# Optimization experiments

Hardware: AMD Instinct MI355X
Metric: run time of the kernel (lower is better)

The kernel has to match this reference:

```python
import jax, jax.numpy as jnp
import numpy as np

B, L = 2048, 8192
IN, H, OUT = 128, 512, 10
N_FRAMES = L // IN  # frame_step == frame_size -> non-overlapping unfold == reshape


def _lstm_layer(xs, W_ih, W_hh, b):
    """xs: [T, B, D_in]; returns (hs [T, B, H], h_T [B, H]).
    PyTorch gate order: i, f, g, o."""
    Bsz = xs.shape[1]
    h0 = jnp.zeros((Bsz, H), xs.dtype)
    c0 = jnp.zeros((Bsz, H), xs.dtype)

    def step(carry, x_t):
        h, c = carry
        gates = x_t @ W_ih.T + h @ W_hh.T + b  # [B, 4H]
        i, f, g, o = jnp.split(gates, 4, axis=-1)
        c = jax.nn.sigmoid(f) * c + jax.nn.sigmoid(i) * jnp.tanh(g)
        h = jax.nn.sigmoid(o) * jnp.tanh(c)
        return (h, c), h

    (hT, _), hs = jax.lax.scan(step, (h0, c0), xs)
    return hs, hT


def setup_inputs() -> dict:
    key = jax.random.key(0)
    ks = jax.random.split(key, 12)
    s_in = 1.0 / np.sqrt(H)
    return {
        "xb": jax.random.normal(ks[0], (B, L), jnp.float32),
        "W_ih0": jax.random.normal(ks[1], (4 * H, IN), jnp.float32) * s_in,
        "W_hh0": jax.random.normal(ks[2], (4 * H, H), jnp.float32) * s_in,
        "b0": jax.random.normal(ks[3], (4 * H,), jnp.float32) * s_in,
        "W_ih1": jax.random.normal(ks[4], (4 * H, H), jnp.float32) * s_in,
        "W_hh1": jax.random.normal(ks[5], (4 * H, H), jnp.float32) * s_in,
        "b1": jax.random.normal(ks[6], (4 * H,), jnp.float32) * s_in,
        "W_out": jax.random.normal(ks[7], (OUT, H), jnp.float32) * s_in,
        "b_out": jax.random.normal(ks[8], (OUT,), jnp.float32) * s_in,
    }


def reference(xb, W_ih0, W_hh0, b0, W_ih1, W_hh1, b1, W_out, b_out):
    # unfold(1, fs, fs) with step==size -> reshape; transpose to time-major
    frames = xb.reshape(B, N_FRAMES, IN).transpose(1, 0, 2)  # [T, B, IN]
    hs0, _ = _lstm_layer(frames, W_ih0, W_hh0, b0)           # [T, B, H]
    _, hT1 = _lstm_layer(hs0, W_ih1, W_hh1, b1)              # [B, H]
    return hT1 @ W_out.T + b_out                             # [B, OUT]
```

## Files before the change

kernel.cpp:

```cpp
#include <hip/hip_runtime.h>
#include <hip/hip_bf16.h>


typedef _Float16 f16x8 __attribute__((ext_vector_type(8)));
typedef float f32x4 __attribute__((ext_vector_type(4)));

#define Bsz 2048
#define Lsz 8192
#define Tsz 64

__global__ void cvt_f32_f16(const float* __restrict__ src, _Float16* __restrict__ dst, int n4) {
    int stride = gridDim.x * blockDim.x;
    for (int i = blockIdx.x * blockDim.x + threadIdx.x; i < n4; i += stride) {
        float4 v = ((const float4*)src)[i];
        union { _Float16 h[4]; ushort4 u; } o;
        o.h[0] = (_Float16)v.x; o.h[1] = (_Float16)v.y;
        o.h[2] = (_Float16)v.z; o.h[3] = (_Float16)v.w;
        ((ushort4*)dst)[i] = o.u;
    }
}

__global__ void pack_w(const float* __restrict__ Wih, const float* __restrict__ Whh,
                       _Float16* __restrict__ dst, int K1) {
    int KT = K1 + 512;
    int n4 = 2048 * KT / 4;
    int stride = gridDim.x * blockDim.x;
    for (int i = blockIdx.x * blockDim.x + threadIdx.x; i < n4; i += stride) {
        int row = i / (KT / 4);
        int col = (i % (KT / 4)) * 4;
        const float* s = (col < K1) ? (Wih + (size_t)row * K1 + col)
                                    : (Whh + (size_t)row * 512 + (col - K1));
        float4 v = *(const float4*)s;
        union { _Float16 h[4]; ushort4 u; } o;
        o.h[0] = (_Float16)v.x; o.h[1] = (_Float16)v.y;
        o.h[2] = (_Float16)v.z; o.h[3] = (_Float16)v.w;
        ((ushort4*)dst)[i] = o.u;
    }
}

__device__ __forceinline__ float fsig(float x)  { return 1.0f / (1.0f + __expf(-x)); }
__device__ __forceinline__ float ftanh(float x) { return 1.0f - 2.0f / (__expf(2.0f * x) + 1.0f); }

template<int K1>
__device__ __forceinline__ void step_tile_lds(
    const _Float16* __restrict__ A1, int lda1,
    const _Float16* __restrict__ A2,
    const _Float16* __restrict__ Wcat,
    const float* __restrict__ bias,
    float* __restrict__ c,
    _Float16* __restrict__ h_out,
    int rowblk, int hcb, char* lA, char* lB)
{
    constexpr int KT  = K1 + 512;
    constexpr int NIT = KT / 64;
    const int tid = threadIdx.x;
    const int ln  = tid & 63;
    const int wv  = tid >> 6;
    const int llo = ln & 15, lhi = ln >> 4;
    const int wx  = wv & 1,  wy  = wv >> 1;
    const int hc0 = hcb * 32;
    const int col = hc0 + wy * 16 + llo;

    const int rsub = ln >> 3;
    const int cg8  = ((ln & 7) ^ rsub) * 8;

    f32x4 acc[4][4] = {};

    float bz[4];
#pragma unroll
    for (int g = 0; g < 4; ++g) bz[g] = bias[512 * g + col];

    for (int it = 0; it < NIT; ++it) {
        const int k0 = it * 64;
#pragma unroll
        for (int q = 0; q < 4; ++q) {
            const int row  = wv * 32 + q * 8 + rsub;
            const int kcol = k0 + cg8;
            const int brow = rowblk * 128 + row;
            const _Float16* srcA = (kcol < K1)
                ? (A1 + (size_t)brow * lda1 + kcol)
                : (A2 + (size_t)brow * 512 + (kcol - K1));
            __builtin_amdgcn_global_load_lds(
                (const __attribute__((address_space(1))) void*)srcA,
                (__attribute__((address_space(3))) void*)(lA + wv * 4096 + q * 1024),
                16, 0, 0);
            const int wrow = ((row >> 5) << 9) + hc0 + (row & 31);
            const _Float16* srcB = Wcat + (size_t)wrow * KT + kcol;
            __builtin_amdgcn_global_load_lds(
                (const __attribute__((address_space(1))) void*)srcB,
                (__attribute__((address_space(3))) void*)(lB + wv * 4096 + q * 1024),
                16, 0, 0);
        }
        __syncthreads();

#pragma unroll
        for (int ks = 0; ks < 2; ++ks) {
            const int gsw = (((ks * 4 + lhi) ^ (llo & 7)) << 4);
            f16x8 a[4], b[4];
#pragma unroll
            for (int mi = 0; mi < 4; ++mi)
                a[mi] = *(const f16x8*)(lA + (wx * 64 + 16 * mi + llo) * 128 + gsw);
#pragma unroll
            for (int g = 0; g < 4; ++g)
                b[g] = *(const f16x8*)(lB + (g * 32 + wy * 16 + llo) * 128 + gsw);
#pragma unroll
            for (int g = 0; g < 4; ++g)
#pragma unroll
                for (int mi = 0; mi < 4; ++mi)
                    acc[g][mi] = __builtin_amdgcn_mfma_f32_16x16x32_f16(
                        a[mi], b[g], acc[g][mi], 0, 0, 0);
        }
        __syncthreads();
    }

#pragma unroll
    for (int mi = 0; mi < 4; ++mi) {
#pragma unroll
        for (int r = 0; r < 4; ++r) {
            const int row = rowblk * 128 + wx * 64 + 16 * mi + lhi * 4 + r;
            float iv = acc[0][mi][r] + bz[0];
            float fv = acc[1][mi][r] + bz[1];
            float gv = acc[2][mi][r] + bz[2];
            float ov = acc[3][mi][r] + bz[3];
            size_t idx = (size_t)row * 512 + col;
            float co = c[idx];
            float cn = fsig(fv) * co + fsig(iv) * ftanh(gv);
            float hn = fsig(ov) * ftanh(cn);
            c[idx] = cn;
            h_out[idx] = (_Float16)hn;
        }
    }
}

__global__ __launch_bounds__(256, 2) void lstm_round(
    int t0, int t1,
    const _Float16* __restrict__ xb16,
    const _Float16* __restrict__ Wc0, const float* __restrict__ b0, float* __restrict__ c0,
    _Float16* __restrict__ h00, _Float16* __restrict__ h01,
    const _Float16* __restrict__ Wc1, const float* __restrict__ b1, float* __restrict__ c1,
    _Float16* __restrict__ h10, _Float16* __restrict__ h11)
{
    __shared__ __align__(16) char lA[16384];
    __shared__ __align__(16) char lB[16384];
    const int bid    = blockIdx.x;
    const int gr     = bid & 7;
    const int rowblk = (bid >> 3) & 15;
    const int gq     = bid >> 7;
    const int grp    = gq * 8 + gr;
    const int hcb    = grp & 15;

    if (grp < 16) {
        if (t0 < 0) return;
        const _Float16* hr = (t0 & 1) ? h01 : h00;
        _Float16*       hw = (t0 & 1) ? h00 : h01;
        step_tile_lds<128>(xb16 + (size_t)t0 * 128, Lsz, hr, Wc0, b0, c0, hw, rowblk, hcb, lA, lB);
    } else {
        if (t1 < 0) return;
        const _Float16* h0in = ((t1 + 1) & 1) ? h01 : h00;
        const _Float16* hr   = (t1 & 1) ? h11 : h10;
        _Float16*       hw   = (t1 & 1) ? h10 : h11;
        step_tile_lds<512>(h0in, 512, hr, Wc1, b1, c1, hw, rowblk, hcb, lA, lB);
    }
}

__global__ void proj_kernel(const _Float16* __restrict__ h1,
                            const float* __restrict__ Wout,
                            const float* __restrict__ bout,
                            float* __restrict__ out)
{
    int tid = blockIdx.x * blockDim.x + threadIdx.x;
    if (tid >= Bsz * 10) return;
    int b = tid / 10, o = tid % 10;
    float s = bout[o];
    const _Float16* hrow = h1 + (size_t)b * 512;
    const float* wrow = Wout + (size_t)o * 512;
    for (int k = 0; k < 512; ++k) s += (float)hrow[k] * wrow[k];
    out[tid] = s;
}

extern "C" void kernel_launch(void* const* d_in, const int* in_sizes, int n_in,
                              void* d_out, int out_size, void* d_ws, size_t ws_size,
                              hipStream_t stream) {
    const float* xb    = (const float*)d_in[0];
    const float* W_ih0 = (const float*)d_in[1];
    const float* W_hh0 = (const float*)d_in[2];
    const float* b0    = (const float*)d_in[3];
    const float* W_ih1 = (const float*)d_in[4];
    const float* W_hh1 = (const float*)d_in[5];
    const float* b1    = (const float*)d_in[6];
    const float* W_out = (const float*)d_in[7];
    const float* b_out = (const float*)d_in[8];
    float* out = (float*)d_out;

    char* ws = (char*)d_ws;
    size_t off = 0;
    auto alloc = [&](size_t bytes) -> void* {
        void* p = ws + off;
        off += (bytes + 255) & ~(size_t)255;
        return p;
    };
    _Float16* xb16 = (_Float16*)alloc((size_t)Bsz * Lsz * 2);
    _Float16* Wc0  = (_Float16*)alloc((size_t)2048 * 640 * 2);
    _Float16* Wc1  = (_Float16*)alloc((size_t)2048 * 1024 * 2);
    _Float16* h00  = (_Float16*)alloc((size_t)Bsz * 512 * 2);
    _Float16* h01  = (_Float16*)alloc((size_t)Bsz * 512 * 2);
    _Float16* h10  = (_Float16*)alloc((size_t)Bsz * 512 * 2);
    _Float16* h11  = (_Float16*)alloc((size_t)Bsz * 512 * 2);
    float* c0 = (float*)alloc((size_t)Bsz * 512 * 4);
    float* c1 = (float*)alloc((size_t)Bsz * 512 * 4);

    cvt_f32_f16<<<2048, 256, 0, stream>>>(xb, xb16, Bsz * Lsz / 4);
    pack_w<<<1280, 256, 0, stream>>>(W_ih0, W_hh0, Wc0, 128);
    pack_w<<<2048, 256, 0, stream>>>(W_ih1, W_hh1, Wc1, 512);

    hipMemsetAsync(h00, 0, (size_t)Bsz * 512 * 2, stream);
    hipMemsetAsync(h10, 0, (size_t)Bsz * 512 * 2, stream);
    hipMemsetAsync(c0, 0, (size_t)Bsz * 512 * 4, stream);
    hipMemsetAsync(c1, 0, (size_t)Bsz * 512 * 4, stream);

    for (int r = 0; r <= Tsz; ++r) {
        int t0 = (r < Tsz) ? r : -1;
        int t1 = r - 1;
        lstm_round<<<dim3(512), 256, 0, stream>>>(t0, t1,
            xb16, Wc0, b0, c0, h00, h01,
            Wc1, b1, c1, h10, h11);
    }

    proj_kernel<<<(Bsz * 10 + 255) / 256, 256, 0, stream>>>(h10, W_out, b_out, out);
}
```

Baseline: 1.784 ms.

## Retile LSTM step to 64x512 blocks with double-buffered LDS and LDS-staged epilogue

Each block now computes a 64-row by 512-gate-column tile (all four gates for 128 hidden units) using 512 threads, instead of 128x128 tiles with 256 threads. K-tile staging is double-buffered in a 144 KB LDS allocation, so the next tile's global loads overlap the current MFMA work. Accumulators go through LDS so the elementwise LSTM cell update reads all four gates per column. The grid drops from 512 to 256 blocks. The large LDS footprint limits residency to one block per CU, and fewer blocks may underfill the GPU.

```diff
diff --git a/kernel.cpp b/kernel.cpp
--- a/kernel.cpp
+++ b/kernel.cpp
@@ -42,97 +42,124 @@
 __device__ __forceinline__ float ftanh(float x) { return 1.0f - 2.0f / (__expf(2.0f * x) + 1.0f); }
 
 template<int K1>
-__device__ __forceinline__ void step_tile_lds(
+__device__ __forceinline__ void stage_tiles(
+    const _Float16* __restrict__ A1, int lda1,
+    const _Float16* __restrict__ A2,
+    const _Float16* __restrict__ Wcat,
+    int grpc, int rowblk, int k0, char* dst, int tid)
+{
+    constexpr int KT = K1 + 512;
+    const int wv = tid >> 6;
+#pragma unroll
+    for (int q = 0; q < 8; ++q) {
+        const int j  = q * 64 + (tid >> 3);
+        const int cg = (((tid & 7) ^ (j & 7)) << 3);
+        const int wrow = ((j >> 7) << 9) + grpc * 128 + (j & 127);
+        const _Float16* src = Wcat + (size_t)wrow * KT + k0 + cg;
+        __builtin_amdgcn_global_load_lds(
+            (const __attribute__((address_space(1))) void*)src,
+            (__attribute__((address_space(3))) void*)(dst + q * 8192 + wv * 1024),
+            16, 0, 0);
+    }
+    {
+        const int row  = tid >> 3;
+        const int cg   = (((tid & 7) ^ (row & 7)) << 3);
+        const int kcol = k0 + cg;
+        const int brow = rowblk * 64 + row;
+        const _Float16* src = (kcol < K1)
+            ? (A1 + (size_t)brow * lda1 + kcol)
+            : (A2 + (size_t)brow * 512 + (kcol - K1));
+        __builtin_amdgcn_global_load_lds(
+            (const __attribute__((address_space(1))) void*)src,
+            (__attribute__((address_space(3))) void*)(dst + 65536 + wv * 1024),
+            16, 0, 0);
+    }
+}
+
+template<int K1>
+__device__ __forceinline__ void step_tile_v5(
     const _Float16* __restrict__ A1, int lda1,
     const _Float16* __restrict__ A2,
     const _Float16* __restrict__ Wcat,
     const float* __restrict__ bias,
     float* __restrict__ c,
     _Float16* __restrict__ h_out,
-    int rowblk, int hcb, char* lA, char* lB)
+    int rowblk, int grpc, char* lds)
 {
     constexpr int KT  = K1 + 512;
     constexpr int NIT = KT / 64;
     const int tid = threadIdx.x;
     const int ln  = tid & 63;
-    const int wv  = tid >> 6;
+    const int wc  = tid >> 6;
     const int llo = ln & 15, lhi = ln >> 4;
-    const int wx  = wv & 1,  wy  = wv >> 1;
-    const int hc0 = hcb * 32;
-    const int col = hc0 + wy * 16 + llo;
-
-    const int rsub = ln >> 3;
-    const int cg8  = ((ln & 7) ^ rsub) * 8;
 
     f32x4 acc[4][4] = {};
 
-    float bz[4];
-#pragma unroll
-    for (int g = 0; g < 4; ++g) bz[g] = bias[512 * g + col];
+    stage_tiles<K1>(A1, lda1, A2, Wcat, grpc, rowblk, 0, lds, tid);
+    __syncthreads();
 
     for (int it = 0; it < NIT; ++it) {
-        const int k0 = it * 64;
-#pragma unroll
-        for (int q = 0; q < 4; ++q) {
-            const int row  = wv * 32 + q * 8 + rsub;
-            const int kcol = k0 + cg8;
-            const int brow = rowblk * 128 + row;
-            const _Float16* srcA = (kcol < K1)
-                ? (A1 + (size_t)brow * lda1 + kcol)
-                : (A2 + (size_t)brow * 512 + (kcol - K1));
-            __builtin_amdgcn_global_load_lds(
-                (const __attribute__((address_space(1))) void*)srcA,
-                (__attribute__((address_space(3))) void*)(lA + wv * 4096 + q * 1024),
-                16, 0, 0);
-            const int wrow = ((row >> 5) << 9) + hc0 + (row & 31);
-            const _Float16* srcB = Wcat + (size_t)wrow * KT + kcol;
-            __builtin_amdgcn_global_load_lds(
-                (const __attribute__((address_space(1))) void*)srcB,
-                (__attribute__((address_space(3))) void*)(lB + wv * 4096 + q * 1024),
-                16, 0, 0);
-        }
-        __syncthreads();
-
+        char* cur = lds + (it & 1) * 73728;
+        if (it + 1 < NIT)
+            stage_tiles<K1>(A1, lda1, A2, Wcat, grpc, rowblk, (it + 1) * 64,
+                            lds + ((it + 1) & 1) * 73728, tid);
 #pragma unroll
         for (int ks = 0; ks < 2; ++ks) {
             const int gsw = (((ks * 4 + lhi) ^ (llo & 7)) << 4);
             f16x8 a[4], b[4];
 #pragma unroll
             for (int mi = 0; mi < 4; ++mi)
-                a[mi] = *(const f16x8*)(lA + (wx * 64 + 16 * mi + llo) * 128 + gsw);
-#pragma unroll
-            for (int g = 0; g < 4; ++g)
-                b[g] = *(const f16x8*)(lB + (g * 32 + wy * 16 + llo) * 128 + gsw);
-#pragma unroll
-            for (int g = 0; g < 4; ++g)
-#pragma unroll
-                for (int mi = 0; mi < 4; ++mi)
-                    acc[g][mi] = __builtin_amdgcn_mfma_f32_16x16x32_f16(
-                        a[mi], b[g], acc[g][mi], 0, 0, 0);
+                a[mi] = *(const f16x8*)(cur + 65536 + (mi * 16 + llo) * 128 + gsw);
+#pragma unroll
+            for (int cf = 0; cf < 4; ++cf)
+                b[cf] = *(const f16x8*)(cur + (wc * 64 + cf * 16 + llo) * 128 + gsw);
+#pragma unroll
+            for (int mi = 0; mi < 4; ++mi)
+#pragma unroll
+                for (int cf = 0; cf < 4; ++cf)
+                    acc[mi][cf] = __builtin_amdgcn_mfma_f32_16x16x32_f16(
+                        a[mi], b[cf], acc[mi][cf], 0, 0, 0);
         }
         __syncthreads();
     }
 
-#pragma unroll
-    for (int mi = 0; mi < 4; ++mi) {
-#pragma unroll
-        for (int r = 0; r < 4; ++r) {
-            const int row = rowblk * 128 + wx * 64 + 16 * mi + lhi * 4 + r;
-            float iv = acc[0][mi][r] + bz[0];
-            float fv = acc[1][mi][r] + bz[1];
-            float gv = acc[2][mi][r] + bz[2];
-            float ov = acc[3][mi][r] + bz[3];
-            size_t idx = (size_t)row * 512 + col;
-            float co = c[idx];
-            float cn = fsig(fv) * co + fsig(iv) * ftanh(gv);
-            float hn = fsig(ov) * ftanh(cn);
-            c[idx] = cn;
-            h_out[idx] = (_Float16)hn;
+    float* gl = (float*)lds;
+#pragma unroll
+    for (int mi = 0; mi < 4; ++mi)
+#pragma unroll
+        for (int cf = 0; cf < 4; ++cf) {
+            const int col = wc * 64 + cf * 16 + llo;
+#pragma unroll
+            for (int r = 0; r < 4; ++r) {
+                const int row = mi * 16 + lhi * 4 + r;
+                gl[row * 512 + col] = acc[mi][cf][r];
+            }
         }
-    }
-}
-
-__global__ __launch_bounds__(256, 2) void lstm_round(
+    __syncthreads();
+
+    const int lc   = tid & 127;
+    const int r0   = tid >> 7;
+    const int hcol = grpc * 128 + lc;
+    float bz[4];
+#pragma unroll
+    for (int g = 0; g < 4; ++g) bz[g] = bias[g * 512 + hcol];
+#pragma unroll
+    for (int i = 0; i < 16; ++i) {
+        const int row = i * 4 + r0;
+        float iv = gl[row * 512 +   0 + lc] + bz[0];
+        float fv = gl[row * 512 + 128 + lc] + bz[1];
+        float gv = gl[row * 512 + 256 + lc] + bz[2];
+        float ov = gl[row * 512 + 384 + lc] + bz[3];
+        const size_t idx = (size_t)(rowblk * 64 + row) * 512 + hcol;
+        float co = c[idx];
+        float cn = fsig(fv) * co + fsig(iv) * ftanh(gv);
+        float hn = fsig(ov) * ftanh(cn);
+        c[idx] = cn;
+        h_out[idx] = (_Float16)hn;
+    }
+}
+
+__global__ __launch_bounds__(512, 2) void lstm_round(
     int t0, int t1,
     const _Float16* __restrict__ xb16,
     const _Float16* __restrict__ Wc0, const float* __restrict__ b0, float* __restrict__ c0,
@@ -140,26 +167,22 @@
     const _Float16* __restrict__ Wc1, const float* __restrict__ b1, float* __restrict__ c1,
     _Float16* __restrict__ h10, _Float16* __restrict__ h11)
 {
-    __shared__ __align__(16) char lA[16384];
-    __shared__ __align__(16) char lB[16384];
+    __shared__ __align__(16) char lds[147456];
     const int bid    = blockIdx.x;
-    const int gr     = bid & 7;
-    const int rowblk = (bid >> 3) & 15;
-    const int gq     = bid >> 7;
-    const int grp    = gq * 8 + gr;
-    const int hcb    = grp & 15;
-
-    if (grp < 16) {
+    const int grp    = bid & 7;
+    const int rowblk = bid >> 3;
+
+    if (grp < 4) {
         if (t0 < 0) return;
         const _Float16* hr = (t0 & 1) ? h01 : h00;
         _Float16*       hw = (t0 & 1) ? h00 : h01;
-        step_tile_lds<128>(xb16 + (size_t)t0 * 128, Lsz, hr, Wc0, b0, c0, hw, rowblk, hcb, lA, lB);
+        step_tile_v5<128>(xb16 + (size_t)t0 * 128, Lsz, hr, Wc0, b0, c0, hw, rowblk, grp, lds);
     } else {
         if (t1 < 0) return;
         const _Float16* h0in = ((t1 + 1) & 1) ? h01 : h00;
         const _Float16* hr   = (t1 & 1) ? h11 : h10;
         _Float16*       hw   = (t1 & 1) ? h10 : h11;
-        step_tile_lds<512>(h0in, 512, hr, Wc1, b1, c1, hw, rowblk, hcb, lA, lB);
+        step_tile_v5<512>(h0in, 512, hr, Wc1, b1, c1, hw, rowblk, grp - 4, lds);
     }
 }
 
@@ -221,7 +244,7 @@
     for (int r = 0; r <= Tsz; ++r) {
         int t0 = (r < Tsz) ? r : -1;
         int t1 = r - 1;
-        lstm_round<<<dim3(512), 256, 0, stream>>>(t0, t1,
+        lstm_round<<<dim3(256), 512, 0, stream>>>(t0, t1,
             xb16, Wc0, b0, c0, h00, h01,
             Wc1, b1, c1, h10, h11);
     }
```

Result: no change. 1.756 ms (-1.6%).
